# Kernel tuning notes

Hardware: AMD Instinct MI355X
Metric: run time of the kernel (lower is better)

Reference implementation:

```python
import jax, jax.numpy as jnp
import numpy as np

N_NODES = 10000
N_EDGES = 320000
IN_CH = 128
HID = 64
HEADS = 8
OUT_CH = 2
NEG_SLOPE = 0.2  # PyG GATConv default
EPS = 1e-16      # PyG softmax denominator eps


def setup_inputs() -> dict:
    key = jax.random.key(0)
    ks = jax.random.split(key, 12)
    x = jax.random.normal(ks[0], (N_NODES, IN_CH), dtype=jnp.float32)
    edge_index = jax.random.randint(ks[1], (2, N_EDGES), 0, N_NODES, dtype=jnp.int64)
    s = 0.05
    W1 = jax.random.normal(ks[2], (IN_CH, HEADS * HID), dtype=jnp.float32) * s
    a_src1 = jax.random.normal(ks[3], (HEADS, HID), dtype=jnp.float32) * s
    a_dst1 = jax.random.normal(ks[4], (HEADS, HID), dtype=jnp.float32) * s
    b1 = jnp.zeros((HEADS * HID,), dtype=jnp.float32)
    W2 = jax.random.normal(ks[5], (HEADS * HID, HID), dtype=jnp.float32) * s
    a_src2 = jax.random.normal(ks[6], (1, HID), dtype=jnp.float32) * s
    a_dst2 = jax.random.normal(ks[7], (1, HID), dtype=jnp.float32) * s
    b2 = jnp.zeros((HID,), dtype=jnp.float32)
    Wc = jax.random.normal(ks[8], (HID, OUT_CH), dtype=jnp.float32) * s
    bc = jnp.zeros((OUT_CH,), dtype=jnp.float32)
    return dict(x=x, edge_index=edge_index, W1=W1, a_src1=a_src1, a_dst1=a_dst1,
                b1=b1, W2=W2, a_src2=a_src2, a_dst2=a_dst2, b2=b2, Wc=Wc, bc=bc)


def gat_layer(x, src, dst, W, a_src, a_dst, bias, heads, ch, concat):
    # x: [N, F_in]; src/dst: [E] (self-loops already appended)
    N = x.shape[0]
    h = (x @ W).reshape(N, heads, ch)                 # [N, H, C]
    e_src = jnp.einsum('nhc,hc->nh', h, a_src)        # [N, H]
    e_dst = jnp.einsum('nhc,hc->nh', h, a_dst)
    e = jax.nn.leaky_relu(e_src[src] + e_dst[dst], NEG_SLOPE)  # [E, H]
    # segment softmax over destination nodes (max-shift has zero gradient)
    m = jax.lax.stop_gradient(jax.ops.segment_max(e, dst, num_segments=N))
    w = jnp.exp(e - m[dst])
    denom = jax.ops.segment_sum(w, dst, num_segments=N)
    alpha = w / (denom[dst] + EPS)                    # [E, H]
    # scatter-aggregate weighted source features
    out = jax.ops.segment_sum(h[src] * alpha[:, :, None], dst, num_segments=N)  # [N,H,C]
    out = out.reshape(N, heads * ch) if concat else out.mean(axis=1)
    return out + bias


def reference(x, edge_index, W1, a_src1, a_dst1, b1, W2, a_src2, a_dst2, b2, Wc, bc):
    N = x.shape[0]
    loop = jnp.arange(N, dtype=edge_index.dtype)
    src = jnp.concatenate([edge_index[0], loop])  # PyG add_self_loops=True
    dst = jnp.concatenate([edge_index[1], loop])
    h1 = gat_layer(x, src, dst, W1, a_src1, a_dst1, b1, HEADS, HID, True)
    h1 = jax.nn.elu(h1)
    # dropout is identity in eval mode
    h2 = gat_layer(h1, src, dst, W2, a_src2, a_dst2, b2, 1, HID, False)
    return h2 @ Wc + bc  # [N, 2]
```

## Files before the change

kernel.cpp:

```cpp
#include <hip/hip_runtime.h>
#include <hip/hip_bf16.h>

#define N_NODES 10000
#define N_EDGES 320000
#define IN_CH 128
#define HID 64
#define HEADS 8
#define OUT_CH 2
#define BM 64
#define BCAP 128
#define MPAD 10048
#define AGG1_BLKS 2048
#define AGG2_BLKS 832

typedef __attribute__((ext_vector_type(8))) short frag8;
typedef __attribute__((ext_vector_type(4))) float f32x4;

__device__ __forceinline__ unsigned short f2bf(float f) {
    union { float f; unsigned u; } v; v.f = f;
    unsigned r = (v.u + 0x7FFFu + ((v.u >> 16) & 1u)) >> 16;
    return (unsigned short)r;
}

__device__ __forceinline__ void g2l16(const void* g, void* l) {
    __builtin_amdgcn_global_load_lds(
        (__attribute__((address_space(1))) unsigned int*)g,
        (__attribute__((address_space(3))) unsigned int*)l, 16, 0, 0);
}

__global__ __launch_bounds__(256) void prep_split(
    const float* __restrict__ x, const float* __restrict__ W1,
    const float* __restrict__ W2,
    unsigned short* __restrict__ xh, unsigned short* __restrict__ xl,
    unsigned short* __restrict__ w1h, unsigned short* __restrict__ w1l,
    unsigned short* __restrict__ w2h, unsigned short* __restrict__ w2l,
    int* __restrict__ cursor) {
    int bx = blockIdx.x, tid = threadIdx.x;
    if (bx < 628) {
        int idx = bx * 256 + tid;
        int row = idx >> 4, c = idx & 15;
        float f[8];
        if (row < N_NODES) {
            float4 v0 = *(const float4*)&x[(size_t)row * IN_CH + c * 8];
            float4 v1 = *(const float4*)&x[(size_t)row * IN_CH + c * 8 + 4];
            f[0] = v0.x; f[1] = v0.y; f[2] = v0.z; f[3] = v0.w;
            f[4] = v1.x; f[5] = v1.y; f[6] = v1.z; f[7] = v1.w;
        } else {
            #pragma unroll
            for (int j = 0; j < 8; j++) f[j] = 0.f;
        }
        unsigned short hb[8], lb[8];
        #pragma unroll
        for (int j = 0; j < 8; j++) {
            hb[j] = f2bf(f[j]);
            float hf = __uint_as_float((unsigned)hb[j] << 16);
            lb[j] = f2bf(f[j] - hf);
        }
        size_t o = ((size_t)row * 16 + (c ^ (row & 15))) * 8;
        *(ushort4*)&xh[o]     = make_ushort4(hb[0], hb[1], hb[2], hb[3]);
        *(ushort4*)&xh[o + 4] = make_ushort4(hb[4], hb[5], hb[6], hb[7]);
        *(ushort4*)&xl[o]     = make_ushort4(lb[0], lb[1], lb[2], lb[3]);
        *(ushort4*)&xl[o + 4] = make_ushort4(lb[4], lb[5], lb[6], lb[7]);
    } else if (bx < 660) {
        int idx = (bx - 628) * 256 + tid;
        int kb = idx >> 9, c = idx & 511;
        int hh = c >> 6, cc = c & 63;
        unsigned short hb[8], lb[8];
        #pragma unroll
        for (int i = 0; i < 8; i++) {
            float v = W1[(size_t)(kb * 8 + i) * (HEADS * HID) + c];
            hb[i] = f2bf(v);
            float hf = __uint_as_float((unsigned)hb[i] << 16);
            lb[i] = f2bf(v - hf);
        }
        size_t o = (((size_t)hh * 16 + kb) * 64 + cc) * 8;
        *(ushort4*)&w1h[o]     = make_ushort4(hb[0], hb[1], hb[2], hb[3]);
        *(ushort4*)&w1h[o + 4] = make_ushort4(hb[4], hb[5], hb[6], hb[7]);
        *(ushort4*)&w1l[o]     = make_ushort4(lb[0], lb[1], lb[2], lb[3]);
        *(ushort4*)&w1l[o + 4] = make_ushort4(lb[4], lb[5], lb[6], lb[7]);
    } else if (bx < 676) {
        int idx = (bx - 660) * 256 + tid;
        int kb = idx >> 6, c = idx & 63;
        unsigned short hb[8], lb[8];
        #pragma unroll
        for (int i = 0; i < 8; i++) {
            float v = W2[(size_t)(kb * 8 + i) * 64 + c];
            hb[i] = f2bf(v);
            float hf = __uint_as_float((unsigned)hb[i] << 16);
            lb[i] = f2bf(v - hf);
        }
        size_t o = ((size_t)kb * 64 + c) * 8;
        *(ushort4*)&w2h[o]     = make_ushort4(hb[0], hb[1], hb[2], hb[3]);
        *(ushort4*)&w2h[o + 4] = make_ushort4(hb[4], hb[5], hb[6], hb[7]);
        *(ushort4*)&w2l[o]     = make_ushort4(lb[0], lb[1], lb[2], lb[3]);
        *(ushort4*)&w2l[o + 4] = make_ushort4(lb[4], lb[5], lb[6], lb[7]);
    } else {
        int idx = (bx - 676) * 256 + tid;
        if (idx < 2500) *(int4*)&cursor[idx * 4] = make_int4(0, 0, 0, 0);
    }
}

__global__ __launch_bounds__(512) void gemm1_fill(
    const unsigned short* __restrict__ xh, const unsigned short* __restrict__ xl,
    const unsigned short* __restrict__ w1h, const unsigned short* __restrict__ w1l,
    const float* __restrict__ a_src1, const float* __restrict__ a_dst1,
    unsigned short* __restrict__ hfeatP,
    float* __restrict__ esAll, float* __restrict__ edAll,
    const int* __restrict__ esrc, const int* __restrict__ edst,
    int* cursor, int* __restrict__ bucket, int M) {
    __shared__ alignas(16) unsigned short Ah[8192];
    __shared__ alignas(16) unsigned short Al[8192];
    __shared__ alignas(16) unsigned short Bh[8192];
    __shared__ alignas(16) unsigned short Bl[8192];
    int tid = threadIdx.x;
    int bxe = blockIdx.x;

    if (tid >= 256) {
        int i = bxe * 256 + (tid - 256);
        if (i < N_EDGES) {
            int d = edst[i];
            int pos = atomicAdd(&cursor[d], 1);
            bucket[(d << 7) + min(pos, BCAP - 1)] = esrc[i];
        }
        __syncthreads();
        __syncthreads();
        __syncthreads();
        return;
    }

    int lane = tid & 63, w = tid >> 6;
    int vb = (bxe & 7) * 157 + (bxe >> 3);
    int h  = vb & 7;
    int bm = (vb >> 3) * BM;

    {
        const unsigned short* gAh = xh  + (size_t)bm * 128;
        const unsigned short* gAl = xl  + (size_t)bm * 128;
        const unsigned short* gBh = w1h + (size_t)h * 8192;
        const unsigned short* gBl = w1l + (size_t)h * 8192;
        #pragma unroll
        for (int i = 0; i < 4; i++) {
            int s = w * 4 + i;
            int go = s * 512 + lane * 8;
            g2l16(gAh + go, &Ah[s * 512]);
            g2l16(gAl + go, &Al[s * 512]);
            g2l16(gBh + go, &Bh[s * 512]);
            g2l16(gBl + go, &Bl[s * 512]);
        }
    }
    __syncthreads();

    int col = lane & 15, g4 = lane >> 4;
    int arow = w * 16 + col;
    f32x4 acc[4] = {};
    #pragma unroll
    for (int ks = 0; ks < 4; ks++) {
        int ai = (arow * 16 + ((ks * 4 + g4) ^ col)) * 8;
        frag8 ah = *(const frag8*)&Ah[ai];
        frag8 al = *(const frag8*)&Al[ai];
        #pragma unroll
        for (int ct = 0; ct < 4; ct++) {
            int bi = ((ks * 4 + g4) * 64 + ct * 16 + col) * 8;
            frag8 bhv = *(const frag8*)&Bh[bi];
            frag8 blv = *(const frag8*)&Bl[bi];
            acc[ct] = __builtin_amdgcn_mfma_f32_16x16x32_bf16(ah, bhv, acc[ct], 0, 0, 0);
            acc[ct] = __builtin_amdgcn_mfma_f32_16x16x32_bf16(al, bhv, acc[ct], 0, 0, 0);
            acc[ct] = __builtin_amdgcn_mfma_f32_16x16x32_bf16(ah, blv, acc[ct], 0, 0, 0);
        }
    }

    float asv[4], adv[4];
    #pragma unroll
    for (int ct = 0; ct < 4; ct++) {
        asv[ct] = a_src1[h * 64 + ct * 16 + col];
        adv[ct] = a_dst1[h * 64 + ct * 16 + col];
    }
    #pragma unroll
    for (int r = 0; r < 4; r++) {
        float s = 0.f, d = 0.f;
        #pragma unroll
        for (int ct = 0; ct < 4; ct++) {
            s += acc[ct][r] * asv[ct];
            d += acc[ct][r] * adv[ct];
        }
        #pragma unroll
        for (int off = 1; off < 16; off <<= 1) {
            s += __shfl_xor(s, off, 64);
            d += __shfl_xor(d, off, 64);
        }
        if (col == 0) {
            int gr = bm + w * 16 + g4 * 4 + r;
            if (gr < M) {
                esAll[(size_t)h * M + gr] = s;
                edAll[(size_t)h * M + gr] = d;
            }
        }
    }

    __syncthreads();
    unsigned short* Tr = Ah;
    int wrow = w * 16 + g4 * 4;
    #pragma unroll
    for (int ct = 0; ct < 4; ct++)
        #pragma unroll
        for (int r = 0; r < 4; r++)
            Tr[(wrow + r) * 68 + ct * 16 + col] = f2bf(acc[ct][r]);
    __syncthreads();
    int row = tid >> 2, q = tid & 3;
    int gr = bm + row;
    if (gr < M) {
        int tb = row * 68 + q * 16;
        ushort4 t0 = *(const ushort4*)&Tr[tb];
        ushort4 t1 = *(const ushort4*)&Tr[tb + 4];
        ushort4 t2 = *(const ushort4*)&Tr[tb + 8];
        ushort4 t3 = *(const ushort4*)&Tr[tb + 12];
        unsigned short* dst =
            &hfeatP[(((size_t)(h >> 1) * M + gr) * 128) + (h & 1) * 64 + q * 16];
        *(ushort4*)&dst[0]  = t0;
        *(ushort4*)&dst[4]  = t1;
        *(ushort4*)&dst[8]  = t2;
        *(ushort4*)&dst[12] = t3;
    }
}

__global__ __launch_bounds__(256) void gemm2_mfma(
    const unsigned short* __restrict__ h1h, const unsigned short* __restrict__ h1l,
    const unsigned short* __restrict__ w2h, const unsigned short* __restrict__ w2l,
    const float* __restrict__ a_src2, const float* __restrict__ a_dst2,
    float* __restrict__ hfeat2, float* __restrict__ es2, float* __restrict__ ed2,
    int M) {
    __shared__ alignas(16) unsigned short Ah[8192];
    __shared__ alignas(16) unsigned short Al[8192];
    __shared__ alignas(16) unsigned short Bh[8192];
    __shared__ alignas(16) unsigned short Bl[8192];
    int tid = threadIdx.x;
    int lane = tid & 63, w = tid >> 6;
    int bm = blockIdx.x * 64;
    int col = lane & 15, g4 = lane >> 4;
    int arow = w * 16 + col;

    f32x4 acc[4] = {};
    for (int t = 0; t < 4; t++) {
        #pragma unroll
        for (int i = 0; i < 4; i++) {
            int s = w * 4 + i;
            int lrow = s * 4 + (lane >> 4);
            int cc = lane & 15;
            int gc = t * 16 + (cc ^ (lrow & 15));
            size_t goA = ((size_t)(bm + lrow) * 64 + gc) * 8;
            g2l16(h1h + goA, &Ah[s * 512]);
            g2l16(h1l + goA, &Al[s * 512]);
            size_t goB = ((size_t)t * 1024 + s * 64 + lane) * 8;
            g2l16(w2h + goB, &Bh[s * 512]);
            g2l16(w2l + goB, &Bl[s * 512]);
        }
        __syncthreads();
        #pragma unroll
        for (int ks = 0; ks < 4; ks++) {
            int ai = (arow * 16 + ((ks * 4 + g4) ^ col)) * 8;
            frag8 ah = *(const frag8*)&Ah[ai];
            frag8 al = *(const frag8*)&Al[ai];
            #pragma unroll
            for (int ct = 0; ct < 4; ct++) {
                int bi = ((ks * 4 + g4) * 64 + ct * 16 + col) * 8;
                frag8 bhv = *(const frag8*)&Bh[bi];
                frag8 blv = *(const frag8*)&Bl[bi];
                acc[ct] = __builtin_amdgcn_mfma_f32_16x16x32_bf16(ah, bhv, acc[ct], 0, 0, 0);
                acc[ct] = __builtin_amdgcn_mfma_f32_16x16x32_bf16(al, bhv, acc[ct], 0, 0, 0);
                acc[ct] = __builtin_amdgcn_mfma_f32_16x16x32_bf16(ah, blv, acc[ct], 0, 0, 0);
            }
        }
        __syncthreads();
    }

    float asv[4], adv[4];
    #pragma unroll
    for (int ct = 0; ct < 4; ct++) {
        asv[ct] = a_src2[ct * 16 + col];
        adv[ct] = a_dst2[ct * 16 + col];
    }
    #pragma unroll
    for (int r = 0; r < 4; r++) {
        int gr = bm + w * 16 + g4 * 4 + r;
        float s = 0.f, d = 0.f;
        #pragma unroll
        for (int ct = 0; ct < 4; ct++) {
            s += acc[ct][r] * asv[ct];
            d += acc[ct][r] * adv[ct];
        }
        #pragma unroll
        for (int off = 1; off < 16; off <<= 1) {
            s += __shfl_xor(s, off, 64);
            d += __shfl_xor(d, off, 64);
        }
        if (gr < M) {
            #pragma unroll
            for (int ct = 0; ct < 4; ct++)
                hfeat2[(size_t)gr * 64 + ct * 16 + col] = acc[ct][r];
            if (col == 0) { es2[gr] = s; ed2[gr] = d; }
        }
    }
}

#define GATH_P(i) {                                                         \
    int b0 = ((i) << 2) + g4;                                               \
    int rbg = __builtin_amdgcn_ds_bpermute(b0, rb);                         \
    float wg = __int_as_float(                                              \
        __builtin_amdgcn_ds_bpermute(b0 + hbaseB, wb));                     \
    const uint4 hv = *(const uint4*)(hptr + rbg);                           \
    a[0] += wg * __uint_as_float(hv.x << 16);                               \
    a[1] += wg * __uint_as_float(hv.x & 0xFFFF0000u);                       \
    a[2] += wg * __uint_as_float(hv.y << 16);                               \
    a[3] += wg * __uint_as_float(hv.y & 0xFFFF0000u);                       \
    a[4] += wg * __uint_as_float(hv.z << 16);                               \
    a[5] += wg * __uint_as_float(hv.z & 0xFFFF0000u);                       \
    a[6] += wg * __uint_as_float(hv.w << 16);                               \
    a[7] += wg * __uint_as_float(hv.w & 0xFFFF0000u);                       \
}

__global__ __launch_bounds__(256) void gat_agg_pair(
    const unsigned short* __restrict__ hfeatP, const float* __restrict__ esAll,
    const float* __restrict__ edAll, const int* __restrict__ bucket,
    const int* __restrict__ cursor, const float* __restrict__ b1,
    unsigned short* __restrict__ h1h, unsigned short* __restrict__ h1l, int M) {
    int bx = blockIdx.x;
    int p = (bx & 7) >> 1;
    int wid = threadIdx.x >> 6;
    int wvp = ((((bx >> 3) << 1) | (bx & 1)) << 2) + wid;
    int l = threadIdx.x & 63;
    int g = l >> 4;
    int q = l & 15;
    int hq = q >> 3;
    int sub = l & 31;
    int hs = l >> 5;
    int g4 = g << 2;
    int hbaseB = hq << 7;
    const char* hptr = (const char*)hfeatP + (size_t)p * M * 256 + (q << 4);
    const float* esS = esAll + (size_t)(p * 2 + hs) * M;
    const float* edS = edAll + (size_t)(p * 2 + hs) * M;

    for (int n = wvp; n < M; n += 2048) {
        float ednS = edS[n];
        int start = n << 7;
        int deg = min(cursor[n], 96);
        int total = deg + 1;

        float a[8] = {};
        float dloc = 0.f;
        for (int base = 0; base < total; base += 32) {
            int idx = base + sub;
            int sld = bucket[start + idx];
            int sv = (idx < deg) ? sld : n;
            float wgt = 0.f;
            if (idx <= deg) {
                float e = esS[sv] + ednS;
                e = (e > 0.f) ? e : 0.2f * e;
                wgt = __expf(e);
            }
            dloc += wgt;
            int rb = sv << 8;
            int wb = __float_as_int(wgt);
            int cnt = min(32, total - base);
            for (int i = 0; i < cnt; i += 4) GATH_P(i)
        }
        #pragma unroll
        for (int off = 16; off; off >>= 1) dloc += __shfl_xor(dloc, off, 64);
        float dother = __shfl_xor(dloc, 32, 64);
        #pragma unroll
        for (int k = 0; k < 8; k++) {
            a[k] += __shfl_xor(a[k], 16, 64);
            a[k] += __shfl_xor(a[k], 32, 64);
        }
        if (g == 0) {
            float d = (hq == 0) ? dloc : dother;
            d += 1e-16f;
            float inv = __builtin_amdgcn_rcpf(d);
            inv = inv * __fmaf_rn(-d, inv, 2.0f);
            const float4 b0v = *(const float4*)&b1[p * 128 + q * 8];
            const float4 b4v = *(const float4*)&b1[p * 128 + q * 8 + 4];
            float vv[8];
            vv[0] = a[0] * inv + b0v.x; vv[1] = a[1] * inv + b0v.y;
            vv[2] = a[2] * inv + b0v.z; vv[3] = a[3] * inv + b0v.w;
            vv[4] = a[4] * inv + b4v.x; vv[5] = a[5] * inv + b4v.y;
            vv[6] = a[6] * inv + b4v.z; vv[7] = a[7] * inv + b4v.w;
            #pragma unroll
            for (int k = 0; k < 8; k++)
                vv[k] = (vv[k] > 0.f) ? vv[k] : (__expf(vv[k]) - 1.f);
            unsigned short hh[8], hl[8];
            #pragma unroll
            for (int k = 0; k < 8; k++) {
                hh[k] = f2bf(vv[k]);
                float hf = __uint_as_float((unsigned)hh[k] << 16);
                hl[k] = f2bf(vv[k] - hf);
            }
            size_t o = ((size_t)n * 64 + p * 16 + q) * 8;
            *(ushort4*)&h1h[o]     = make_ushort4(hh[0], hh[1], hh[2], hh[3]);
            *(ushort4*)&h1h[o + 4] = make_ushort4(hh[4], hh[5], hh[6], hh[7]);
            *(ushort4*)&h1l[o]     = make_ushort4(hl[0], hl[1], hl[2], hl[3]);
            *(ushort4*)&h1l[o + 4] = make_ushort4(hl[4], hl[5], hl[6], hl[7]);
        }
    }
}

#define GATH_2(i) {                                                         \
    int bidx = ((i) << 2) + g4;                                             \
    int rbg = __builtin_amdgcn_ds_bpermute(bidx, rb);                       \
    float wg = __int_as_float(__builtin_amdgcn_ds_bpermute(bidx, wb));      \
    const float4 hv = *(const float4*)((const char*)hfeat2 + (rbg + qoff)); \
    ax += wg * hv.x;                                                        \
    ay += wg * hv.y;                                                        \
    az += wg * hv.z;                                                        \
    aw += wg * hv.w;                                                        \
}

__global__ __launch_bounds__(256) void gat_agg2(
    const float* __restrict__ hfeat2, const float* __restrict__ es,
    const float* __restrict__ ed, const int* __restrict__ bucket,
    const int* __restrict__ cursor, const float* __restrict__ b2,
    const float* __restrict__ Wc, const float* __restrict__ bc,
    float* __restrict__ out) {
    int wv = blockIdx.x * 4 + (threadIdx.x >> 6);
    int l = threadIdx.x & 63;
    int g = l >> 4;
    int q = l & 15;
    int g4 = g << 2;
    int qoff = q << 4;

    for (int n = wv; n < N_NODES; n += AGG2_BLKS * 4) {
        int start = n << 7;
        int deg = min(cursor[n], 96);
        int total = deg + 1;
        float edn = ed[n];

        float ax = 0.f, ay = 0.f, az = 0.f, aw = 0.f;
        float dloc = 0.f;
        for (int base = 0; base < total; base += 64) {
            int cnt = min(64, total - base);
            float wgt = 0.f;
            int sv = n;
            if (l < cnt) {
                int idx = base + l;
                sv = (idx < deg) ? bucket[start + idx] : n;
                float e = es[sv] + edn;
                e = (e > 0.f) ? e : 0.2f * e;
                wgt = __expf(e);
            }
            dloc += wgt;
            int rb = sv << 8;
            int wb = __float_as_int(wgt);
            for (int i = 0; i < cnt; i += 4) GATH_2(i)
        }
        float d = dloc;
        #pragma unroll
        for (int off = 32; off; off >>= 1) d += __shfl_down(d, off, 64);
        d = __shfl(d, 0, 64) + 1e-16f;
        float inv = __builtin_amdgcn_rcpf(d);
        inv = inv * __fmaf_rn(-d, inv, 2.0f);
        ax += __shfl_down(ax, 32, 64); ay += __shfl_down(ay, 32, 64);
        az += __shfl_down(az, 32, 64); aw += __shfl_down(aw, 32, 64);
        ax += __shfl_down(ax, 16, 64); ay += __shfl_down(ay, 16, 64);
        az += __shfl_down(az, 16, 64); aw += __shfl_down(aw, 16, 64);
        float p0 = 0.f, p1 = 0.f;
        if (g == 0) {
            const float4 bq = *(const float4*)&b2[q * 4];
            float h0 = ax * inv + bq.x, h1v = ay * inv + bq.y;
            float h2v = az * inv + bq.z, h3 = aw * inv + bq.w;
            const float2* WcV = (const float2*)Wc;
            float2 w0 = WcV[q * 4 + 0], w1 = WcV[q * 4 + 1];
            float2 w2 = WcV[q * 4 + 2], w3 = WcV[q * 4 + 3];
            p0 = h0 * w0.x + h1v * w1.x + h2v * w2.x + h3 * w3.x;
            p1 = h0 * w0.y + h1v * w1.y + h2v * w2.y + h3 * w3.y;
        }
        #pragma unroll
        for (int off = 1; off < 16; off <<= 1) {
            p0 += __shfl_xor(p0, off, 64);
            p1 += __shfl_xor(p1, off, 64);
        }
        if (l == 0) {
            out[n * 2 + 0] = p0 + bc[0];
            out[n * 2 + 1] = p1 + bc[1];
        }
    }
}

extern "C" void kernel_launch(void* const* d_in, const int* in_sizes, int n_in,
                              void* d_out, int out_size, void* d_ws, size_t ws_size,
                              hipStream_t stream) {
    const float* x      = (const float*)d_in[0];
    const int*   eidx   = (const int*)d_in[1];
    const float* W1     = (const float*)d_in[2];
    const float* a_src1 = (const float*)d_in[3];
    const float* a_dst1 = (const float*)d_in[4];
    const float* b1     = (const float*)d_in[5];
    const float* W2     = (const float*)d_in[6];
    const float* a_src2 = (const float*)d_in[7];
    const float* a_dst2 = (const float*)d_in[8];
    const float* b2     = (const float*)d_in[9];
    const float* Wc     = (const float*)d_in[10];
    const float* bc     = (const float*)d_in[11];
    float* out = (float*)d_out;

    const int N = N_NODES, E = N_EDGES;
    const int* esrc = eidx;
    const int* edst = eidx + E;

    size_t off = 0;
    auto alloc = [&](size_t bytes) {
        void* p = (char*)d_ws + off;
        off += (bytes + 255) & ~(size_t)255;
        return p;
    };
    int*   cursor   = (int*)alloc((size_t)N * 4);
    int*   bucket   = (int*)alloc((size_t)N * BCAP * 4);
    unsigned short* hfeatP = (unsigned short*)alloc((size_t)4 * N * 128 * 2);
    unsigned short* h1h = (unsigned short*)alloc((size_t)MPAD * 512 * 2);
    unsigned short* h1l = (unsigned short*)alloc((size_t)MPAD * 512 * 2);
    float* hfeat2   = (float*)alloc((size_t)N * 64 * 4);
    float* esAll    = (float*)alloc((size_t)HEADS * N * 4);
    float* edAll    = (float*)alloc((size_t)HEADS * N * 4);
    float* es2      = (float*)alloc((size_t)N * 4);
    float* ed2      = (float*)alloc((size_t)N * 4);
    unsigned short* xh  = (unsigned short*)alloc((size_t)MPAD * 128 * 2);
    unsigned short* xl  = (unsigned short*)alloc((size_t)MPAD * 128 * 2);
    unsigned short* w1h = (unsigned short*)alloc((size_t)128 * 512 * 2);
    unsigned short* w1l = (unsigned short*)alloc((size_t)128 * 512 * 2);
    unsigned short* w2h = (unsigned short*)alloc((size_t)512 * 64 * 2);
    unsigned short* w2l = (unsigned short*)alloc((size_t)512 * 64 * 2);

    prep_split<<<686, 256, 0, stream>>>(x, W1, W2, xh, xl, w1h, w1l, w2h, w2l,
                                        cursor);
    gemm1_fill<<<157 * 8, 512, 0, stream>>>(
        xh, xl, w1h, w1l, a_src1, a_dst1, hfeatP, esAll, edAll,
        esrc, edst, cursor, bucket, N);
    gat_agg_pair<<<AGG1_BLKS, 256, 0, stream>>>(hfeatP, esAll, edAll,
                                                bucket, cursor, b1, h1h, h1l, N);
    gemm2_mfma<<<157, 256, 0, stream>>>(h1h, h1l, w2h, w2l, a_src2, a_dst2,
                                        hfeat2, es2, ed2, N);
    gat_agg2<<<AGG2_BLKS, 256, 0, stream>>>(hfeat2, es2, ed2, bucket, cursor,
                                            b2, Wc, bc, out);
}
```

Baseline: 169.7 us.

## Software-pipeline edge chunk loads across nodes in layer-1 aggregation

Restructures the per-node aggregation loop in gat_agg_pair into a flat chunk stream that prefetches bucket indices two chunks ahead and source scores one chunk ahead, including across node boundaries. Cursor and destination scores for upcoming nodes are also loaded early. This hides the dependent index-then-score-then-gather latency chain. The cost is more live registers, more complex control flow, and an extra state machine for node transitions.

```diff
diff --git a/kernel.cpp b/kernel.cpp
--- a/kernel.cpp
+++ b/kernel.cpp
@@ -321,8 +321,9 @@
 __global__ __launch_bounds__(256) void gat_agg_pair(
     const unsigned short* __restrict__ hfeatP, const float* __restrict__ esAll,
     const float* __restrict__ edAll, const int* __restrict__ bucket,
-    const int* __restrict__ cursor, const float* __restrict__ b1,
+    const int* __restrict__ cursor, const float* __restrict__ b1_,
     unsigned short* __restrict__ h1h, unsigned short* __restrict__ h1l, int M) {
+    const int S = 2048;
     int bx = blockIdx.x;
     int p = (bx & 7) >> 1;
     int wid = threadIdx.x >> 6;
@@ -339,66 +340,115 @@
     const float* esS = esAll + (size_t)(p * 2 + hs) * M;
     const float* edS = edAll + (size_t)(p * 2 + hs) * M;
 
-    for (int n = wvp; n < M; n += 2048) {
-        float ednS = edS[n];
-        int start = n << 7;
-        int deg = min(cursor[n], 96);
-        int total = deg + 1;
-
-        float a[8] = {};
-        float dloc = 0.f;
-        for (int base = 0; base < total; base += 32) {
-            int idx = base + sub;
-            int sld = bucket[start + idx];
-            int sv = (idx < deg) ? sld : n;
-            float wgt = 0.f;
-            if (idx <= deg) {
-                float e = esS[sv] + ednS;
-                e = (e > 0.f) ? e : 0.2f * e;
-                wgt = __expf(e);
-            }
-            dloc += wgt;
-            int rb = sv << 8;
-            int wb = __float_as_int(wgt);
-            int cnt = min(32, total - base);
+    int nc = wvp;
+    int totc = min(cursor[nc], 96) + 1;
+    float ednc = edS[nc];
+    int nN = nc + S;
+    int cur1 = (nN < M) ? cursor[nN] : 0;
+    float edn1m = (nN < M) ? edS[nN] : 0.f;
+    int nN2 = nc + 2 * S;
+    int cur2 = (nN2 < M) ? cursor[nN2] : 0;
+    float edn2m = (nN2 < M) ? edS[nN2] : 0.f;
+
+    float dlA, dlB = 0.f;
+    int rb_c, wb_c;
+    {
+        int degc = totc - 1;
+        int sld = bucket[(nc << 7) + sub];
+        int sv = (sub < degc) ? sld : nc;
+        float wgt = 0.f;
+        if (sub <= degc) {
+            float e = esS[sv] + ednc;
+            e = (e > 0.f) ? e : 0.2f * e;
+            wgt = __expf(e);
+        }
+        dlA = wgt; rb_c = sv << 8; wb_c = __float_as_int(wgt);
+    }
+    int bc = 0;
+    int n1, b1;
+    if (32 < totc) { n1 = nc; b1 = 32; } else { n1 = nN; b1 = 0; }
+    int sld1 = 0;
+    if (n1 < M) sld1 = bucket[(n1 << 7) + b1 + sub];
+
+    float a[8] = {};
+    while (true) {
+        int tot1 = (n1 == nc) ? totc : (min(cur1, 96) + 1);
+        int n2, b2;
+        if (b1 + 32 < tot1) { n2 = n1; b2 = b1 + 32; }
+        else { n2 = (n1 == nc) ? nN : (nN + S); b2 = 0; }
+        int sld2 = 0;
+        if (n2 < M) sld2 = bucket[(n2 << 7) + b2 + sub];
+        int deg1 = tot1 - 1;
+        int idx1 = b1 + sub;
+        int sv1 = (idx1 < deg1) ? sld1 : n1;
+        float es1 = 0.f;
+        if (n1 < M) es1 = esS[sv1];
+        {
+            int cnt = min(32, totc - bc);
+            int rb = rb_c, wb = wb_c;
             for (int i = 0; i < cnt; i += 4) GATH_P(i)
         }
-        #pragma unroll
-        for (int off = 16; off; off >>= 1) dloc += __shfl_xor(dloc, off, 64);
-        float dother = __shfl_xor(dloc, 32, 64);
-        #pragma unroll
-        for (int k = 0; k < 8; k++) {
-            a[k] += __shfl_xor(a[k], 16, 64);
-            a[k] += __shfl_xor(a[k], 32, 64);
-        }
-        if (g == 0) {
-            float d = (hq == 0) ? dloc : dother;
-            d += 1e-16f;
-            float inv = __builtin_amdgcn_rcpf(d);
-            inv = inv * __fmaf_rn(-d, inv, 2.0f);
-            const float4 b0v = *(const float4*)&b1[p * 128 + q * 8];
-            const float4 b4v = *(const float4*)&b1[p * 128 + q * 8 + 4];
-            float vv[8];
-            vv[0] = a[0] * inv + b0v.x; vv[1] = a[1] * inv + b0v.y;
-            vv[2] = a[2] * inv + b0v.z; vv[3] = a[3] * inv + b0v.w;
-            vv[4] = a[4] * inv + b4v.x; vv[5] = a[5] * inv + b4v.y;
-            vv[6] = a[6] * inv + b4v.z; vv[7] = a[7] * inv + b4v.w;
+        float edn1v = (n1 == nc) ? ednc : edn1m;
+        float w1 = 0.f;
+        if (n1 < M && idx1 <= deg1) {
+            float e = es1 + edn1v;
+            e = (e > 0.f) ? e : 0.2f * e;
+            w1 = __expf(e);
+        }
+        if (n1 == nc) dlA += w1; else dlB += w1;
+
+        if (n1 != nc) {
+            float dloc = dlA;
             #pragma unroll
-            for (int k = 0; k < 8; k++)
-                vv[k] = (vv[k] > 0.f) ? vv[k] : (__expf(vv[k]) - 1.f);
-            unsigned short hh[8], hl[8];
+            for (int off = 16; off; off >>= 1) dloc += __shfl_xor(dloc, off, 64);
+            float dother = __shfl_xor(dloc, 32, 64);
             #pragma unroll
             for (int k = 0; k < 8; k++) {
-                hh[k] = f2bf(vv[k]);
-                float hf = __uint_as_float((unsigned)hh[k] << 16);
-                hl[k] = f2bf(vv[k] - hf);
+                a[k] += __shfl_xor(a[k], 16, 64);
+                a[k] += __shfl_xor(a[k], 32, 64);
             }
-            size_t o = ((size_t)n * 64 + p * 16 + q) * 8;
-            *(ushort4*)&h1h[o]     = make_ushort4(hh[0], hh[1], hh[2], hh[3]);
-            *(ushort4*)&h1h[o + 4] = make_ushort4(hh[4], hh[5], hh[6], hh[7]);
-            *(ushort4*)&h1l[o]     = make_ushort4(hl[0], hl[1], hl[2], hl[3]);
-            *(ushort4*)&h1l[o + 4] = make_ushort4(hl[4], hl[5], hl[6], hl[7]);
-        }
+            if (g == 0) {
+                float d = (hq == 0) ? dloc : dother;
+                d += 1e-16f;
+                float inv = __builtin_amdgcn_rcpf(d);
+                inv = inv * __fmaf_rn(-d, inv, 2.0f);
+                const float4 b0v = *(const float4*)&b1_[p * 128 + q * 8];
+                const float4 b4v = *(const float4*)&b1_[p * 128 + q * 8 + 4];
+                float vv[8];
+                vv[0] = a[0] * inv + b0v.x; vv[1] = a[1] * inv + b0v.y;
+                vv[2] = a[2] * inv + b0v.z; vv[3] = a[3] * inv + b0v.w;
+                vv[4] = a[4] * inv + b4v.x; vv[5] = a[5] * inv + b4v.y;
+                vv[6] = a[6] * inv + b4v.z; vv[7] = a[7] * inv + b4v.w;
+                #pragma unroll
+                for (int k = 0; k < 8; k++)
+                    vv[k] = (vv[k] > 0.f) ? vv[k] : (__expf(vv[k]) - 1.f);
+                unsigned short hh[8], hl[8];
+                #pragma unroll
+                for (int k = 0; k < 8; k++) {
+                    hh[k] = f2bf(vv[k]);
+                    float hf = __uint_as_float((unsigned)hh[k] << 16);
+                    hl[k] = f2bf(vv[k] - hf);
+                }
+                size_t o = ((size_t)nc * 64 + p * 16 + q) * 8;
+                *(ushort4*)&h1h[o]     = make_ushort4(hh[0], hh[1], hh[2], hh[3]);
+                *(ushort4*)&h1h[o + 4] = make_ushort4(hh[4], hh[5], hh[6], hh[7]);
+                *(ushort4*)&h1l[o]     = make_ushort4(hl[0], hl[1], hl[2], hl[3]);
+                *(ushort4*)&h1l[o + 4] = make_ushort4(hl[4], hl[5], hl[6], hl[7]);
+            }
+            if (n1 >= M) return;
+            nc = n1; totc = min(cur1, 96) + 1; ednc = edn1m;
+            nN = nc + S;
+            cur1 = cur2; edn1m = edn2m;
+            nN2 = nc + 2 * S;
+            cur2 = (nN2 < M) ? cursor[nN2] : 0;
+            edn2m = (nN2 < M) ? edS[nN2] : 0.f;
+            dlA = dlB; dlB = 0.f;
+            #pragma unroll
+            for (int k = 0; k < 8; k++) a[k] = 0.f;
+        }
+        bc = b1;
+        rb_c = sv1 << 8; wb_c = __float_as_int(w1);
+        sld1 = sld2; n1 = n2; b1 = b2;
     }
 }
 
```

Result: no change. 168.8 us, median of 2 (-0.6%).
